# Kernel tuning notes

Hardware: AMD Instinct MI355X
Metric: run time of the kernel (lower is better)

The kernel has to match this reference:

```python
import jax, jax.numpy as jnp
import numpy as np

B, D, H, O, E = 16384, 1024, 512, 256, 8


def setup_inputs() -> dict:
    key = jax.random.key(0)
    ks = jax.random.split(key, 8)
    s = lambda k, shape, fan: (jax.random.normal(k, shape, jnp.float32) / np.sqrt(fan).astype(np.float32))
    z = lambda shape: jnp.zeros(shape, jnp.float32)
    return {
        "x": jax.random.normal(ks[0], (B, D), jnp.float32),
        # gating network: D -> 256 -> 128 -> E
        "gw1": s(ks[1], (D, 256), D), "gb1": z((256,)),
        "gw2": s(ks[2], (256, 128), 256), "gb2": z((128,)),
        "gw3": s(ks[3], (128, E), 128), "gb3": z((E,)),
        # experts, batched over expert dim E: D -> H -> H -> O
        "ew1": s(ks[4], (E, D, H), D), "eb1": z((E, H)),
        "ew2": s(ks[5], (E, H, H), H), "eb2": z((E, H)),
        "ew3": s(ks[6], (E, H, O), H), "eb3": z((E, O)),
    }


def reference(x, gw1, gb1, gw2, gb2, gw3, gb3, ew1, eb1, ew2, eb2, ew3, eb3):
    # Gating network (dropout is identity in eval mode)
    g = jax.nn.relu(x @ gw1 + gb1)
    g = jax.nn.relu(g @ gw2 + gb2)
    gates = jax.nn.softmax(g @ gw3 + gb3, axis=1)  # [B, E]
    # All experts run on every token: batched small MLPs over expert axis e
    h = jax.nn.relu(jnp.einsum('bd,edh->ebh', x, ew1) + eb1[:, None, :])   # [E, B, H]
    h = jax.nn.relu(jnp.einsum('ebh,ehk->ebk', h, ew2) + eb2[:, None, :])  # [E, B, H]
    eo = jnp.einsum('ebh,eho->ebo', h, ew3) + eb3[:, None, :]              # [E, B, O]
    # gate-weighted sum over experts
    out = jnp.einsum('ebo,be->bo', eo, gates)  # [B, O]
    return out
```

## Files before the change

kernel.cpp:

```cpp
#include <hip/hip_runtime.h>
#include <hip/hip_bf16.h>

typedef __hip_bfloat16 bf16;
typedef __attribute__((ext_vector_type(8))) __bf16 bf16x8;
typedef __attribute__((ext_vector_type(4))) float f32x4;

#define B_ 16384
#define D_ 1024
#define H_ 512
#define O_ 256
#define E_ 8
#define BC_ 8192

static_assert(B_ % BC_ == 0, "chunking");

#define GLDS(src, dst) __builtin_amdgcn_global_load_lds( \
    (const __attribute__((address_space(1))) void*)(src), \
    (__attribute__((address_space(3))) void*)(dst), 16, 0, 0)

#define BAR()   asm volatile("s_barrier" ::: "memory")
#define LGKM0() do { asm volatile("s_waitcnt lgkmcnt(0)" ::: "memory"); \
                     __builtin_amdgcn_sched_barrier(0); } while (0)

__global__ void detect_k(const unsigned short* __restrict__ x, int* __restrict__ flag) {
    __shared__ int s;
    if (threadIdx.x == 0) s = 0;
    __syncthreads();
    int big = 0;
    for (int i = threadIdx.x; i < 2048; i += 256)
        if (((x[i] >> 7) & 0xFF) >= 150) big = 1;
    if (big) atomicOr(&s, 1);
    __syncthreads();
    if (threadIdx.x == 0) *flag = s;
}

__global__ void cvt_k(const void* __restrict__ src, bf16* __restrict__ dst,
                      const int* __restrict__ flag, long n) {
    const int f = *flag;
    long i = (long)blockIdx.x * blockDim.x + threadIdx.x;
    const long stride = (long)gridDim.x * blockDim.x;
    if (f) {
        const float* s = (const float*)src;
        for (; i < n; i += stride) dst[i] = __float2bfloat16(s[i]);
    } else {
        const bf16* s = (const bf16*)src;
        for (; i < n; i += stride) dst[i] = s[i];
    }
}

__global__ void transpose_k(const void* __restrict__ in, bf16* __restrict__ out,
                            const int* __restrict__ flag, int R, int C,
                            long z_out, long c_stride) {
    __shared__ bf16 t[32][33];
    const int f = *flag;
    const long zi = (long)blockIdx.z * R * C;
    const int x = blockIdx.x * 32 + threadIdx.x;
    const int y0 = blockIdx.y * 32;
    const float* inf = (const float*)in;
    const bf16* inb = (const bf16*)in;
#pragma unroll
    for (int i = 0; i < 4; i++) {
        int r = y0 + threadIdx.y + i * 8;
        long idx = zi + (long)r * C + x;
        t[threadIdx.y + i * 8][threadIdx.x] =
            f ? __float2bfloat16(inf[idx]) : inb[idx];
    }
    __syncthreads();
    const int xr = blockIdx.y * 32 + threadIdx.x;
    const long zo = (long)blockIdx.z * z_out;
#pragma unroll
    for (int i = 0; i < 4; i++) {
        int c = blockIdx.x * 32 + threadIdx.y + i * 8;
        out[zo + (long)c * c_stride + xr] = t[threadIdx.x][threadIdx.y + i * 8];
    }
}

__global__ void gate3_softmax_k(const bf16* __restrict__ g2,
                                const bf16* __restrict__ gw3,
                                const bf16* __restrict__ gb3,
                                float* __restrict__ gates) {
    __shared__ float w[128 * 8];
    __shared__ float bsh[8];
    const int tid = threadIdx.x;
    for (int i = tid; i < 1024; i += 256) w[i] = __bfloat162float(gw3[i]);
    if (tid < 8) bsh[tid] = __bfloat162float(gb3[tid]);
    __syncthreads();

    const long row = (long)blockIdx.x * 256 + tid;
    float acc[8];
#pragma unroll
    for (int o = 0; o < 8; o++) acc[o] = bsh[o];

    const bf16x8* rp8 = (const bf16x8*)(g2 + row * 128);
#pragma unroll 4
    for (int c8 = 0; c8 < 16; c8++) {
        bf16x8 v8 = rp8[c8];
#pragma unroll
        for (int jj = 0; jj < 8; jj++) {
            float v = (float)v8[jj];
            int k = c8 * 8 + jj;
#pragma unroll
            for (int o = 0; o < 8; o++) acc[o] += v * w[k * 8 + o];
        }
    }
    float m = acc[0];
#pragma unroll
    for (int o = 1; o < 8; o++) m = fmaxf(m, acc[o]);
    float s = 0.f;
#pragma unroll
    for (int o = 0; o < 8; o++) { acc[o] = __expf(acc[o] - m); s += acc[o]; }
    const float inv = 1.f / s;
#pragma unroll
    for (int o = 0; o < 8; o++) gates[row * 8 + o] = acc[o] * inv;
}

template <int MODE>
__global__ __launch_bounds__(256, 4)
void gemm_bt(const bf16* __restrict__ A, const bf16* __restrict__ Bt,
             const bf16* __restrict__ bias, const float* __restrict__ gates,
             void* __restrict__ Cout, const bf16* __restrict__ eb3,
             const int* __restrict__ oflag,
             int lda, int ldb, int ldo, int K,
             long a_z, long b_z, long bias_z, long out_z,
             int e_gate, int k_per_e, long a_e, long b_e, long row0) {
    __shared__ __attribute__((aligned(16))) bf16 As[128 * 32];
    __shared__ __attribute__((aligned(16))) bf16 Bs[128 * 32];

    const int tid  = threadIdx.x;
    const int lane = tid & 63;
    const int quad = lane >> 4;
    const int l15  = lane & 15;
    const int wid  = tid >> 6;
    const int wr   = (wid >> 1) << 6;
    const int wc   = (wid & 1) << 6;
    const int z    = blockIdx.z;
    const long m0  = (long)blockIdx.y << 7;
    const long n0  = (long)blockIdx.x << 7;

    const bf16* Az = A + (long)z * a_z;
    const bf16* Bz = Bt + (long)z * b_z;

    f32x4 acc[4][4];
#pragma unroll
    for (int i = 0; i < 4; i++)
#pragma unroll
        for (int j = 0; j < 4; j++) acc[i][j] = (f32x4){0.f, 0.f, 0.f, 0.f};

    const int erow = tid >> 2;
    const int ecol = (tid & 3) << 3;

    const int n_e   = k_per_e ? (K / k_per_e) : 1;
    const int inner = (k_per_e ? k_per_e : K) >> 5;

    for (int e = 0; e < n_e; e++) {
        const bf16* Ae = Az + (long)e * a_e;
        const bf16* Be = Bz + (long)e * b_e;
        for (int kti = 0; kti < inner; kti++) {
            const int kk = kti << 5;
#pragma unroll
            for (int i = 0; i < 2; i++) {
                const int r = (i << 6) + erow;
                GLDS(Ae + (m0 + r) * lda + (kk + ecol), As + r * 32 + ecol);
            }
#pragma unroll
            for (int i = 0; i < 2; i++) {
                const int r = (i << 6) + erow;
                GLDS(Be + (n0 + r) * ldb + (kk + ecol), Bs + r * 32 + ecol);
            }
            __syncthreads();
            bf16x8 af[4], bfr[4];
#pragma unroll
            for (int i = 0; i < 4; i++)
                af[i] = *(const bf16x8*)(As + (wr + i * 16 + l15) * 32 + (quad << 3));
#pragma unroll
            for (int j = 0; j < 4; j++)
                bfr[j] = *(const bf16x8*)(Bs + (wc + j * 16 + l15) * 32 + (quad << 3));
#pragma unroll
            for (int i = 0; i < 4; i++)
#pragma unroll
                for (int j = 0; j < 4; j++)
                    acc[i][j] = __builtin_amdgcn_mfma_f32_16x16x32_bf16(
                        af[i], bfr[j], acc[i][j], 0, 0, 0);
            __syncthreads();
        }
    }

    const int eg = (e_gate >= 0) ? e_gate : z;

    if constexpr (MODE == 0 || MODE == 1) {
        bf16* C = (bf16*)Cout + (long)z * out_z;
        const bf16* bb = bias + (long)z * bias_z;
        float gv[4][4];
        if constexpr (MODE == 1) {
#pragma unroll
            for (int i = 0; i < 4; i++)
#pragma unroll
                for (int rg = 0; rg < 4; rg++)
                    gv[i][rg] = gates[(row0 + m0 + wr + i * 16 + quad * 4 + rg) * 8 + eg];
        }
#pragma unroll
        for (int j = 0; j < 4; j++) {
            const int c = (int)n0 + wc + j * 16 + l15;
            const float bv = __bfloat162float(bb[c]);
#pragma unroll
            for (int i = 0; i < 4; i++) {
#pragma unroll
                for (int rg = 0; rg < 4; rg++) {
                    const long r = m0 + wr + i * 16 + quad * 4 + rg;
                    float v = fmaxf(acc[i][j][rg] + bv, 0.f);
                    if constexpr (MODE == 1) v *= gv[i][rg];
                    C[r * ldo + c] = __float2bfloat16(v);
                }
            }
        }
    } else if constexpr (MODE == 2) {
        float* C = (float*)Cout;
#pragma unroll
        for (int i = 0; i < 4; i++) {
#pragma unroll
            for (int rg = 0; rg < 4; rg++) {
                const long r = m0 + wr + i * 16 + quad * 4 + rg;
                const float g = gates[(row0 + r) * 8 + eg];
#pragma unroll
                for (int j = 0; j < 4; j++) {
                    const int c = (int)n0 + wc + j * 16 + l15;
                    const float b3 = __bfloat162float(eb3[eg * O_ + c]);
                    C[r * ldo + c] += acc[i][j][rg] + g * b3;
                }
            }
        }
    }
}

template <int MODE>
__global__ __launch_bounds__(512, 2)
void gemm256(const bf16* __restrict__ A, const bf16* __restrict__ Bt,
             const bf16* __restrict__ bias, const float* __restrict__ gates,
             void* __restrict__ Cout, const bf16* __restrict__ eb3,
             int lda, int ldb, int ldo, int K,
             long a_z, long b_z, long bias_z, long out_z, long row0) {
    __shared__ __attribute__((aligned(16))) bf16 lds[2][2][256 * 64];

    int bx = blockIdx.x, by = blockIdx.y;
    {
        const int gx = gridDim.x;
        const int nwg = gx * gridDim.y;
        if ((nwg & 7) == 0) {
            int lin = bx + gx * by;
            lin = (lin & 7) * (nwg >> 3) + (lin >> 3);
            bx = lin % gx; by = lin / gx;
        }
    }

    const int tid  = threadIdx.x;
    const int lane = tid & 63;
    const int quad = lane >> 4;
    const int l15  = lane & 15;
    const int w    = tid >> 6;
    const int wm   = w >> 2;
    const int wn   = w & 3;
    const int z    = blockIdx.z;
    const long m0  = (long)by << 8;
    const long n0  = (long)bx << 8;

    const bf16* __restrict__ Az = A + z * a_z;
    const bf16* __restrict__ Bz = Bt + z * b_z;

    f32x4 acc[8][4];
#pragma unroll
    for (int i = 0; i < 8; ++i)
#pragma unroll
        for (int j = 0; j < 4; ++j) acc[i][j] = (f32x4){0.f, 0.f, 0.f, 0.f};

    bf16x8 af[4][2], bv[2][2];

    auto stage = [&](int buf, int mat, int half, int kt) {
        const bf16* __restrict__ G = mat ? Bz : Az;
        const int ld = mat ? ldb : lda;
        const long p0 = mat ? n0 : m0;
#pragma unroll
        for (int l = 0; l < 2; ++l) {
            const int ci = (w << 1) | l;
            const int rb = mat ? ((ci >> 2) << 6) + (half << 5) + ((ci & 3) << 3)
                               : ((ci >> 3) << 7) + (half << 6) + ((ci & 7) << 3);
            const int row = rb + (lane >> 3);
            const int cb  = ((lane & 7) << 4) ^ ((row & 7) << 4);
            GLDS(G + (p0 + row) * ld + kt * 64 + (cb >> 1),
                 &lds[buf][mat][rb * 64]);
        }
    };
    auto ldaf = [&](int buf, int qm) {
#pragma unroll
        for (int i = 0; i < 4; ++i) {
            const int r = (wm << 7) + (qm << 6) + (i << 4) + l15;
            const char* p = (const char*)&lds[buf][0][r * 64];
            const int sw = (r & 7) << 4;
#pragma unroll
            for (int s = 0; s < 2; ++s)
                af[i][s] = *(const bf16x8*)(p + (((s << 6) + (quad << 4)) ^ sw));
        }
    };
    auto ldbf = [&](int buf, int qn) {
#pragma unroll
        for (int j = 0; j < 2; ++j) {
            const int r = (wn << 6) + (qn << 5) + (j << 4) + l15;
            const char* p = (const char*)&lds[buf][1][r * 64];
            const int sw = (r & 7) << 4;
#pragma unroll
            for (int s = 0; s < 2; ++s)
                bv[j][s] = *(const bf16x8*)(p + (((s << 6) + (quad << 4)) ^ sw));
        }
    };
    auto mmac = [&](int qm, int qn) {
#pragma unroll
        for (int i = 0; i < 4; ++i)
#pragma unroll
            for (int j = 0; j < 2; ++j)
#pragma unroll
                for (int s = 0; s < 2; ++s)
                    acc[(qm << 2) + i][(qn << 1) + j] =
                        __builtin_amdgcn_mfma_f32_16x16x32_bf16(
                            af[i][s], bv[j][s], acc[(qm << 2) + i][(qn << 1) + j],
                            0, 0, 0);
    };

    const int nt = K >> 6;

    stage(0, 0, 0, 0); stage(0, 0, 1, 0); stage(0, 1, 0, 0); stage(0, 1, 1, 0);
    stage(1, 0, 0, 1); stage(1, 1, 0, 1);
    asm volatile("s_waitcnt vmcnt(4)" ::: "memory");
    BAR();

    const int hi = nt >> 1;
    for (int it = 0; it < hi; ++it) {
        const int t1k = 2 * it + 1, t2k = 2 * it + 2, t3k = 2 * it + 3;
        const bool do2 = t2k < nt, do3 = t3k < nt;
        ldaf(0, 0); ldbf(0, 0); stage(1, 0, 1, t1k);
        BAR(); LGKM0();
        __builtin_amdgcn_s_setprio(1); mmac(0, 0); __builtin_amdgcn_s_setprio(0);
        BAR();
        ldbf(0, 1); stage(1, 1, 1, t1k);
        BAR(); LGKM0();
        __builtin_amdgcn_s_setprio(1); mmac(0, 1); __builtin_amdgcn_s_setprio(0);
        BAR();
        ldaf(0, 1); ldbf(0, 0); if (do2) stage(0, 0, 0, t2k);
        BAR(); LGKM0();
        __builtin_amdgcn_s_setprio(1); mmac(1, 0); __builtin_amdgcn_s_setprio(0);
        BAR();
        ldbf(0, 1); if (do2) stage(0, 1, 0, t2k);
        BAR(); LGKM0();
        __builtin_amdgcn_s_setprio(1); mmac(1, 1); __builtin_amdgcn_s_setprio(0);
        if (do2) { asm volatile("s_waitcnt vmcnt(4)" ::: "memory"); }
        else     { asm volatile("s_waitcnt vmcnt(0)" ::: "memory"); }
        BAR();
        ldaf(1, 0); ldbf(1, 0); if (do2) stage(0, 0, 1, t2k);
        BAR(); LGKM0();
        __builtin_amdgcn_s_setprio(1); mmac(0, 0); __builtin_amdgcn_s_setprio(0);
        BAR();
        ldbf(1, 1); if (do2) stage(0, 1, 1, t2k);
        BAR(); LGKM0();
        __builtin_amdgcn_s_setprio(1); mmac(0, 1); __builtin_amdgcn_s_setprio(0);
        BAR();
        ldaf(1, 1); ldbf(1, 0); if (do3) stage(1, 0, 0, t3k);
        BAR(); LGKM0();
        __builtin_amdgcn_s_setprio(1); mmac(1, 0); __builtin_amdgcn_s_setprio(0);
        BAR();
        ldbf(1, 1); if (do3) stage(1, 1, 0, t3k);
        BAR(); LGKM0();
        __builtin_amdgcn_s_setprio(1); mmac(1, 1); __builtin_amdgcn_s_setprio(0);
        if (do3) { asm volatile("s_waitcnt vmcnt(4)" ::: "memory"); }
        else     { asm volatile("s_waitcnt vmcnt(0)" ::: "memory"); }
        BAR();
    }

    if constexpr (MODE == 0 || MODE == 1) {
        bf16* C = (bf16*)Cout + z * out_z;
        const bf16* bb = bias + z * bias_z;
        float bvv[4];
#pragma unroll
        for (int jg = 0; jg < 4; ++jg)
            bvv[jg] = __bfloat162float(bb[(int)n0 + (wn << 6) + (jg << 4) + l15]);
#pragma unroll
        for (int ig = 0; ig < 8; ++ig) {
#pragma unroll
            for (int rg = 0; rg < 4; ++rg) {
                const long r = m0 + (wm << 7) + (ig << 4) + (quad << 2) + rg;
                float g = 1.f;
                if constexpr (MODE == 1) g = gates[(row0 + r) * 8 + z];
#pragma unroll
                for (int jg = 0; jg < 4; ++jg) {
                    const int c = (int)n0 + (wn << 6) + (jg << 4) + l15;
                    float v = fmaxf(acc[ig][jg][rg] + bvv[jg], 0.f);
                    if constexpr (MODE == 1) v *= g;
                    C[r * ldo + c] = __float2bfloat16(v);
                }
            }
        }
    } else {
        float* C = (float*)Cout + z * out_z;
        float b3v[4];
#pragma unroll
        for (int jg = 0; jg < 4; ++jg)
            b3v[jg] = __bfloat162float(eb3[z * O_ + (int)n0 + (wn << 6) + (jg << 4) + l15]);
#pragma unroll
        for (int ig = 0; ig < 8; ++ig) {
#pragma unroll
            for (int rg = 0; rg < 4; ++rg) {
                const long r = m0 + (wm << 7) + (ig << 4) + (quad << 2) + rg;
                const float g = gates[(row0 + r) * 8 + z];
#pragma unroll
                for (int jg = 0; jg < 4; ++jg) {
                    const int c = (int)n0 + (wn << 6) + (jg << 4) + l15;
                    C[r * ldo + c] = acc[ig][jg][rg] + g * b3v[jg];
                }
            }
        }
    }
}

__global__ void zero_f32_k(float* __restrict__ p) {
    p[(long)blockIdx.x * 256 + threadIdx.x] = 0.f;
}
__global__ void out_cvt_k(const float* __restrict__ in, void* __restrict__ out,
                          const int* __restrict__ flag) {
    const long i = (long)blockIdx.x * 256 + threadIdx.x;
    if (*flag) ((float*)out)[i] = in[i];
    else       ((bf16*)out)[i] = __float2bfloat16(in[i]);
}
__global__ void reduce8_k(const float* __restrict__ p, void* __restrict__ out,
                          const int* __restrict__ flag, long off) {
    const long n = (long)BC_ * O_;
    const long i = ((long)blockIdx.x * 256 + threadIdx.x) * 4;
    float4 s = *(const float4*)(p + i);
#pragma unroll
    for (int zz = 1; zz < 8; ++zz) {
        float4 a = *(const float4*)(p + (long)zz * n + i);
        s.x += a.x; s.y += a.y; s.z += a.z; s.w += a.w;
    }
    if (*flag) {
        *(float4*)((float*)out + off + i) = s;
    } else {
        bf16* o = (bf16*)out + off + i;
        o[0] = __float2bfloat16(s.x); o[1] = __float2bfloat16(s.y);
        o[2] = __float2bfloat16(s.z); o[3] = __float2bfloat16(s.w);
    }
}

extern "C" void kernel_launch(void* const* d_in, const int* in_sizes, int n_in,
                              void* d_out, int out_size, void* d_ws, size_t ws_size,
                              hipStream_t stream) {
    (void)in_sizes; (void)n_in; (void)out_size;
    const void* x   = d_in[0];
    const void* gw1 = d_in[1];
    const void* gb1 = d_in[2];
    const void* gw2 = d_in[3];
    const void* gb2 = d_in[4];
    const void* gw3 = d_in[5];
    const void* gb3 = d_in[6];
    const void* ew1 = d_in[7];
    const void* eb1 = d_in[8];
    const void* ew2 = d_in[9];
    const void* eb2 = d_in[10];
    const void* ew3 = d_in[11];
    const void* eb3 = d_in[12];

    char* ws = (char*)d_ws;
    size_t off = 0;
    auto alloc = [&](size_t n) { char* p = ws + off; off += (n + 255) & ~(size_t)255; return p; };

    int*  flag  = (int*)alloc(256);
    bf16* xc    = (bf16*)alloc((size_t)B_ * D_ * 2);
    bf16* gw1t  = (bf16*)alloc((size_t)256 * 1024 * 2);
    bf16* gw2t  = (bf16*)alloc((size_t)128 * 256 * 2);
    bf16* ew1t  = (bf16*)alloc((size_t)E_ * H_ * D_ * 2);
    bf16* ew2t  = (bf16*)alloc((size_t)E_ * H_ * H_ * 2);
    bf16* ew3t  = (bf16*)alloc((size_t)E_ * O_ * H_ * 2);
    bf16* gb1c  = (bf16*)alloc(256 * 2);
    bf16* gb2c  = (bf16*)alloc(128 * 2);
    bf16* gw3c  = (bf16*)alloc(1024 * 2);
    bf16* gb3c  = (bf16*)alloc(8 * 2);
    bf16* eb1c  = (bf16*)alloc((size_t)E_ * H_ * 2);
    bf16* eb2c  = (bf16*)alloc((size_t)E_ * H_ * 2);
    bf16* eb3c  = (bf16*)alloc((size_t)E_ * O_ * 2);
    bf16* g1    = (bf16*)alloc((size_t)B_ * 256 * 2);
    bf16* g2b   = (bf16*)alloc((size_t)B_ * 128 * 2);
    float* gates = (float*)alloc((size_t)B_ * 8 * 4);

    const size_t small = off;
    const size_t needA = small + ((size_t)E_ * BC_ * H_ * 2 + 256)
                               + ((size_t)BC_ * E_ * H_ * 2 + 256)
                               + (8ull * BC_ * O_ * 4 + 256) + 4096;
    const bool pathA = ws_size >= needA;

    detect_k<<<1, 256, 0, stream>>>((const unsigned short*)x, flag);

    cvt_k<<<4096, 256, 0, stream>>>(x, xc, flag, (long)B_ * D_);
    cvt_k<<<1, 256, 0, stream>>>(gb1, gb1c, flag, 256);
    cvt_k<<<1, 256, 0, stream>>>(gb2, gb2c, flag, 128);
    cvt_k<<<4, 256, 0, stream>>>(gw3, gw3c, flag, 1024);
    cvt_k<<<1, 256, 0, stream>>>(gb3, gb3c, flag, 8);
    cvt_k<<<16, 256, 0, stream>>>(eb1, eb1c, flag, (long)E_ * H_);
    cvt_k<<<16, 256, 0, stream>>>(eb2, eb2c, flag, (long)E_ * H_);
    cvt_k<<<8, 256, 0, stream>>>(eb3, eb3c, flag, (long)E_ * O_);

    transpose_k<<<dim3(256 / 32, 1024 / 32, 1), dim3(32, 8), 0, stream>>>(
        gw1, gw1t, flag, 1024, 256, 0L, 1024L);
    transpose_k<<<dim3(128 / 32, 256 / 32, 1), dim3(32, 8), 0, stream>>>(
        gw2, gw2t, flag, 256, 128, 0L, 256L);
    transpose_k<<<dim3(H_ / 32, D_ / 32, E_), dim3(32, 8), 0, stream>>>(
        ew1, ew1t, flag, D_, H_, (long)H_ * D_, (long)D_);
    transpose_k<<<dim3(H_ / 32, H_ / 32, E_), dim3(32, 8), 0, stream>>>(
        ew2, ew2t, flag, H_, H_, (long)H_ * H_, (long)H_);
    if (pathA)
        transpose_k<<<dim3(O_ / 32, H_ / 32, E_), dim3(32, 8), 0, stream>>>(
            ew3, ew3t, flag, H_, O_, (long)H_, (long)E_ * H_);
    else
        transpose_k<<<dim3(O_ / 32, H_ / 32, E_), dim3(32, 8), 0, stream>>>(
            ew3, ew3t, flag, H_, O_, (long)O_ * H_, (long)H_);

    gemm_bt<0><<<dim3(2, 128, 1), 256, 0, stream>>>(
        xc, gw1t, gb1c, nullptr, g1, nullptr, nullptr,
        1024, 1024, 256, 1024, 0, 0, 0, 0, 0, 0, 0, 0, 0);
    gemm_bt<0><<<dim3(1, 128, 1), 256, 0, stream>>>(
        g1, gw2t, gb2c, nullptr, g2b, nullptr, nullptr,
        256, 256, 128, 256, 0, 0, 0, 0, 0, 0, 0, 0, 0);
    gate3_softmax_k<<<dim3(B_ / 256), 256, 0, stream>>>(g2b, gw3c, gb3c, gates);

    if (pathA) {
        bf16* h1c   = (bf16*)alloc((size_t)E_ * BC_ * H_ * 2);
        bf16* h2    = (bf16*)alloc((size_t)BC_ * E_ * H_ * 2);
        float* parts = (float*)alloc(8ull * BC_ * O_ * 4);
        for (int ch = 0; ch < B_ / BC_; ch++) {
            const long rb = (long)ch * BC_;
            gemm256<0><<<dim3(2, BC_ / 256, 8), 512, 0, stream>>>(
                xc + rb * D_, ew1t, eb1c, nullptr, h1c, nullptr,
                D_, D_, H_, D_,
                0, (long)H_ * D_, (long)H_, (long)BC_ * H_, 0);
            gemm256<1><<<dim3(2, BC_ / 256, 8), 512, 0, stream>>>(
                h1c, ew2t, eb2c, gates, h2, nullptr,
                H_, H_, E_ * H_, H_,
                (long)BC_ * H_, (long)H_ * H_, (long)H_, (long)H_, rb);
            gemm256<4><<<dim3(1, BC_ / 256, 8), 512, 0, stream>>>(
                h2, ew3t, nullptr, gates, parts, eb3c,
                E_ * H_, E_ * H_, O_, 512,
                (long)H_, (long)H_, 0, (long)BC_ * O_, rb);
            reduce8_k<<<dim3(BC_ * O_ / 1024), 256, 0, stream>>>(
                parts, d_out, flag, rb * O_);
        }
    } else {
        bf16* h1s = (bf16*)alloc((size_t)B_ * H_ * 2);
        bf16* h2s = (bf16*)alloc((size_t)B_ * H_ * 2);
        float* oacc = (float*)alloc((size_t)B_ * O_ * 4);
        zero_f32_k<<<dim3(B_ * O_ / 256), 256, 0, stream>>>(oacc);
        for (int e = 0; e < E_; e++) {
            gemm_bt<0><<<dim3(4, 128, 1), 256, 0, stream>>>(
                xc, ew1t + (size_t)e * H_ * D_, eb1c + (size_t)e * H_, nullptr, h1s, nullptr, nullptr,
                1024, 1024, 512, 1024, 0, 0, 0, 0, 0, 0, 0, 0, 0);
            gemm_bt<1><<<dim3(4, 128, 1), 256, 0, stream>>>(
                h1s, ew2t + (size_t)e * H_ * H_, eb2c + (size_t)e * H_, gates, h2s, nullptr, nullptr,
                512, 512, 512, 512, 0, 0, 0, 0, e, 0, 0, 0, 0);
            gemm_bt<2><<<dim3(2, 128, 1), 256, 0, stream>>>(
                h2s, ew3t + (size_t)e * O_ * H_, nullptr, gates, oacc, eb3c, nullptr,
                512, 512, 256, 512, 0, 0, 0, 0, e, 0, 0, 0, 0);
        }
        out_cvt_k<<<dim3(B_ * O_ / 256), 256, 0, stream>>>(oacc, d_out, flag);
    }
}
```

Before: 547.7 us.

## Fuse pairs of experts per GEMM block and batch layer-3 across chunks

The expert GEMM kernel now walks several expert segments along K in one launch, running a per-segment epilogue mid-loop. Each block handles two experts, so the grid z-dimension is halved for layers 1 and 2. When workspace allows, layer 3 runs once over the full batch with four partial outputs and a 4-way reduce instead of per-chunk 8-way partials. The small conversion kernels are merged into one launch and the x conversion is vectorised. This cuts launch count, partial-sum traffic and reduce work, at the cost of extra epilogue work inside the main loop and larger h2 and parts buffers.

```diff
diff --git a/kernel.cpp b/kernel.cpp
--- a/kernel.cpp
+++ b/kernel.cpp
@@ -34,18 +34,44 @@
     if (threadIdx.x == 0) *flag = s;
 }
 
-__global__ void cvt_k(const void* __restrict__ src, bf16* __restrict__ dst,
-                      const int* __restrict__ flag, long n) {
+__global__ void cvtx_k(const void* __restrict__ src, bf16* __restrict__ dst,
+                       const int* __restrict__ flag, long n8) {
     const int f = *flag;
     long i = (long)blockIdx.x * blockDim.x + threadIdx.x;
     const long stride = (long)gridDim.x * blockDim.x;
     if (f) {
-        const float* s = (const float*)src;
-        for (; i < n; i += stride) dst[i] = __float2bfloat16(s[i]);
+        const float4* s = (const float4*)src;
+        for (; i < n8; i += stride) {
+            float4 a = s[2 * i], b = s[2 * i + 1];
+            bf16 tmp[8];
+            tmp[0] = __float2bfloat16(a.x); tmp[1] = __float2bfloat16(a.y);
+            tmp[2] = __float2bfloat16(a.z); tmp[3] = __float2bfloat16(a.w);
+            tmp[4] = __float2bfloat16(b.x); tmp[5] = __float2bfloat16(b.y);
+            tmp[6] = __float2bfloat16(b.z); tmp[7] = __float2bfloat16(b.w);
+            *(uint4*)(dst + i * 8) = *(const uint4*)tmp;
+        }
     } else {
-        const bf16* s = (const bf16*)src;
-        for (; i < n; i += stride) dst[i] = s[i];
-    }
+        const uint4* s = (const uint4*)src;
+        for (; i < n8; i += stride) *(uint4*)(dst + i * 8) = s[i];
+    }
+}
+
+__global__ void small_cvt_k(const void* s0, const void* s1, const void* s2,
+                            const void* s3, const void* s4, const void* s5,
+                            const void* s6,
+                            bf16* d0, bf16* d1, bf16* d2, bf16* d3,
+                            bf16* d4, bf16* d5, bf16* d6,
+                            const int* __restrict__ flag) {
+    const int f = *flag;
+    const int id = blockIdx.x;
+    const void* sp[7] = {s0, s1, s2, s3, s4, s5, s6};
+    bf16* dp[7] = {d0, d1, d2, d3, d4, d5, d6};
+    const int len[7] = {256, 128, 1024, 8, E_ * H_, E_ * H_, E_ * O_};
+    const float* sf = (const float*)sp[id];
+    const bf16*  sb = (const bf16*)sp[id];
+    bf16* d = dp[id];
+    for (int i = threadIdx.x; i < len[id]; i += 256)
+        d[i] = f ? __float2bfloat16(sf[i]) : sb[i];
 }
 
 __global__ void transpose_k(const void* __restrict__ in, bf16* __restrict__ out,
@@ -237,8 +263,9 @@
 void gemm256(const bf16* __restrict__ A, const bf16* __restrict__ Bt,
              const bf16* __restrict__ bias, const float* __restrict__ gates,
              void* __restrict__ Cout, const bf16* __restrict__ eb3,
-             int lda, int ldb, int ldo, int K,
-             long a_z, long b_z, long bias_z, long out_z, long row0) {
+             int lda, int ldb, int ldo, int nseg, int ksh,
+             long a_z, long a_s, long b_e, long bias_e,
+             long out_e, long out_z, long row0) {
     __shared__ __attribute__((aligned(16))) bf16 lds[2][2][256 * 64];
 
     int bx = blockIdx.x, by = blockIdx.y;
@@ -263,9 +290,6 @@
     const long m0  = (long)by << 8;
     const long n0  = (long)bx << 8;
 
-    const bf16* __restrict__ Az = A + z * a_z;
-    const bf16* __restrict__ Bz = Bt + z * b_z;
-
     f32x4 acc[8][4];
 #pragma unroll
     for (int i = 0; i < 8; ++i)
@@ -274,8 +298,16 @@
 
     bf16x8 af[4][2], bv[2][2];
 
+    const int ntseg = 1 << ksh;
+    const int nt    = nseg << ksh;
+    const int seghi = 1 << (ksh - 1);
+
     auto stage = [&](int buf, int mat, int half, int kt) {
-        const bf16* __restrict__ G = mat ? Bz : Az;
+        const int seg = kt >> ksh;
+        const int ktl = kt & (ntseg - 1);
+        const long e  = (long)z * nseg + seg;
+        const bf16* __restrict__ G =
+            mat ? (Bt + e * b_e) : (A + (long)z * a_z + (long)seg * a_s);
         const int ld = mat ? ldb : lda;
         const long p0 = mat ? n0 : m0;
 #pragma unroll
@@ -285,7 +317,7 @@
                                : ((ci >> 3) << 7) + (half << 6) + ((ci & 7) << 3);
             const int row = rb + (lane >> 3);
             const int cb  = ((lane & 7) << 4) ^ ((row & 7) << 4);
-            GLDS(G + (p0 + row) * ld + kt * 64 + (cb >> 1),
+            GLDS(G + (p0 + row) * ld + ktl * 64 + (cb >> 1),
                  &lds[buf][mat][rb * 64]);
         }
     };
@@ -323,59 +355,10 @@
                             af[i][s], bv[j][s], acc[(qm << 2) + i][(qn << 1) + j],
                             0, 0, 0);
     };
-
-    const int nt = K >> 6;
-
-    stage(0, 0, 0, 0); stage(0, 0, 1, 0); stage(0, 1, 0, 0); stage(0, 1, 1, 0);
-    stage(1, 0, 0, 1); stage(1, 1, 0, 1);
-    asm volatile("s_waitcnt vmcnt(4)" ::: "memory");
-    BAR();
-
-    const int hi = nt >> 1;
-    for (int it = 0; it < hi; ++it) {
-        const int t1k = 2 * it + 1, t2k = 2 * it + 2, t3k = 2 * it + 3;
-        const bool do2 = t2k < nt, do3 = t3k < nt;
-        ldaf(0, 0); ldbf(0, 0); stage(1, 0, 1, t1k);
-        BAR(); LGKM0();
-        __builtin_amdgcn_s_setprio(1); mmac(0, 0); __builtin_amdgcn_s_setprio(0);
-        BAR();
-        ldbf(0, 1); stage(1, 1, 1, t1k);
-        BAR(); LGKM0();
-        __builtin_amdgcn_s_setprio(1); mmac(0, 1); __builtin_amdgcn_s_setprio(0);
-        BAR();
-        ldaf(0, 1); ldbf(0, 0); if (do2) stage(0, 0, 0, t2k);
-        BAR(); LGKM0();
-        __builtin_amdgcn_s_setprio(1); mmac(1, 0); __builtin_amdgcn_s_setprio(0);
-        BAR();
-        ldbf(0, 1); if (do2) stage(0, 1, 0, t2k);
-        BAR(); LGKM0();
-        __builtin_amdgcn_s_setprio(1); mmac(1, 1); __builtin_amdgcn_s_setprio(0);
-        if (do2) { asm volatile("s_waitcnt vmcnt(4)" ::: "memory"); }
-        else     { asm volatile("s_waitcnt vmcnt(0)" ::: "memory"); }
-        BAR();
-        ldaf(1, 0); ldbf(1, 0); if (do2) stage(0, 0, 1, t2k);
-        BAR(); LGKM0();
-        __builtin_amdgcn_s_setprio(1); mmac(0, 0); __builtin_amdgcn_s_setprio(0);
-        BAR();
-        ldbf(1, 1); if (do2) stage(0, 1, 1, t2k);
-        BAR(); LGKM0();
-        __builtin_amdgcn_s_setprio(1); mmac(0, 1); __builtin_amdgcn_s_setprio(0);
-        BAR();
-        ldaf(1, 1); ldbf(1, 0); if (do3) stage(1, 0, 0, t3k);
-        BAR(); LGKM0();
-        __builtin_amdgcn_s_setprio(1); mmac(1, 0); __builtin_amdgcn_s_setprio(0);
-        BAR();
-        ldbf(1, 1); if (do3) stage(1, 1, 0, t3k);
-        BAR(); LGKM0();
-        __builtin_amdgcn_s_setprio(1); mmac(1, 1); __builtin_amdgcn_s_setprio(0);
-        if (do3) { asm volatile("s_waitcnt vmcnt(4)" ::: "memory"); }
-        else     { asm volatile("s_waitcnt vmcnt(0)" ::: "memory"); }
-        BAR();
-    }
-
-    if constexpr (MODE == 0 || MODE == 1) {
-        bf16* C = (bf16*)Cout + z * out_z;
-        const bf16* bb = bias + z * bias_z;
+    auto epi01 = [&](int s) {
+        const long e = (long)z * nseg + s;
+        bf16* C = (bf16*)Cout + e * out_e;
+        const bf16* bb = bias + e * bias_e;
         float bvv[4];
 #pragma unroll
         for (int jg = 0; jg < 4; ++jg)
@@ -386,7 +369,7 @@
             for (int rg = 0; rg < 4; ++rg) {
                 const long r = m0 + (wm << 7) + (ig << 4) + (quad << 2) + rg;
                 float g = 1.f;
-                if constexpr (MODE == 1) g = gates[(row0 + r) * 8 + z];
+                if constexpr (MODE == 1) g = gates[(row0 + r) * 8 + e];
 #pragma unroll
                 for (int jg = 0; jg < 4; ++jg) {
                     const int c = (int)n0 + (wn << 6) + (jg << 4) + l15;
@@ -396,22 +379,84 @@
                 }
             }
         }
+#pragma unroll
+        for (int i = 0; i < 8; ++i)
+#pragma unroll
+            for (int j = 0; j < 4; ++j) acc[i][j] = (f32x4){0.f, 0.f, 0.f, 0.f};
+    };
+
+    stage(0, 0, 0, 0); stage(0, 0, 1, 0); stage(0, 1, 0, 0); stage(0, 1, 1, 0);
+    stage(1, 0, 0, 1); stage(1, 1, 0, 1);
+    asm volatile("s_waitcnt vmcnt(4)" ::: "memory");
+    BAR();
+
+    const int hi = nt >> 1;
+    for (int it = 0; it < hi; ++it) {
+        const int t1k = 2 * it + 1, t2k = 2 * it + 2, t3k = 2 * it + 3;
+        const bool do2 = t2k < nt, do3 = t3k < nt;
+        ldaf(0, 0); ldbf(0, 0); stage(1, 0, 1, t1k);
+        BAR(); LGKM0();
+        __builtin_amdgcn_s_setprio(1); mmac(0, 0); __builtin_amdgcn_s_setprio(0);
+        BAR();
+        ldbf(0, 1); stage(1, 1, 1, t1k);
+        BAR(); LGKM0();
+        __builtin_amdgcn_s_setprio(1); mmac(0, 1); __builtin_amdgcn_s_setprio(0);
+        BAR();
+        ldaf(0, 1); ldbf(0, 0); if (do2) stage(0, 0, 0, t2k);
+        BAR(); LGKM0();
+        __builtin_amdgcn_s_setprio(1); mmac(1, 0); __builtin_amdgcn_s_setprio(0);
+        BAR();
+        ldbf(0, 1); if (do2) stage(0, 1, 0, t2k);
+        BAR(); LGKM0();
+        __builtin_amdgcn_s_setprio(1); mmac(1, 1); __builtin_amdgcn_s_setprio(0);
+        if (do2) { asm volatile("s_waitcnt vmcnt(4)" ::: "memory"); }
+        else     { asm volatile("s_waitcnt vmcnt(0)" ::: "memory"); }
+        BAR();
+        ldaf(1, 0); ldbf(1, 0); if (do2) stage(0, 0, 1, t2k);
+        BAR(); LGKM0();
+        __builtin_amdgcn_s_setprio(1); mmac(0, 0); __builtin_amdgcn_s_setprio(0);
+        BAR();
+        ldbf(1, 1); if (do2) stage(0, 1, 1, t2k);
+        BAR(); LGKM0();
+        __builtin_amdgcn_s_setprio(1); mmac(0, 1); __builtin_amdgcn_s_setprio(0);
+        BAR();
+        ldaf(1, 1); ldbf(1, 0); if (do3) stage(1, 0, 0, t3k);
+        BAR(); LGKM0();
+        __builtin_amdgcn_s_setprio(1); mmac(1, 0); __builtin_amdgcn_s_setprio(0);
+        BAR();
+        ldbf(1, 1); if (do3) stage(1, 1, 0, t3k);
+        BAR(); LGKM0();
+        __builtin_amdgcn_s_setprio(1); mmac(1, 1); __builtin_amdgcn_s_setprio(0);
+        if (do3) { asm volatile("s_waitcnt vmcnt(4)" ::: "memory"); }
+        else     { asm volatile("s_waitcnt vmcnt(0)" ::: "memory"); }
+        BAR();
+        if constexpr (MODE == 0 || MODE == 1) {
+            if (nseg > 1 && ((it + 1) & (seghi - 1)) == 0) {
+                const int s = ((it + 1) >> (ksh - 1)) - 1;
+                if (s < nseg - 1) epi01(s);
+            }
+        }
+    }
+
+    if constexpr (MODE == 0 || MODE == 1) {
+        epi01(nseg - 1);
     } else {
-        float* C = (float*)Cout + z * out_z;
-        float b3v[4];
-#pragma unroll
-        for (int jg = 0; jg < 4; ++jg)
-            b3v[jg] = __bfloat162float(eb3[z * O_ + (int)n0 + (wn << 6) + (jg << 4) + l15]);
+        float* C = (float*)Cout + (long)z * out_z;
 #pragma unroll
         for (int ig = 0; ig < 8; ++ig) {
 #pragma unroll
             for (int rg = 0; rg < 4; ++rg) {
                 const long r = m0 + (wm << 7) + (ig << 4) + (quad << 2) + rg;
-                const float g = gates[(row0 + r) * 8 + z];
 #pragma unroll
                 for (int jg = 0; jg < 4; ++jg) {
                     const int c = (int)n0 + (wn << 6) + (jg << 4) + l15;
-                    C[r * ldo + c] = acc[ig][jg][rg] + g * b3v[jg];
+                    float v = acc[ig][jg][rg];
+                    for (int s = 0; s < nseg; ++s) {
+                        const long e = (long)z * nseg + s;
+                        v += gates[(row0 + r) * 8 + e] *
+                             __bfloat162float(eb3[e * O_ + c]);
+                    }
+                    C[r * ldo + c] = v;
                 }
             }
         }
@@ -427,13 +472,13 @@
     if (*flag) ((float*)out)[i] = in[i];
     else       ((bf16*)out)[i] = __float2bfloat16(in[i]);
 }
-__global__ void reduce8_k(const float* __restrict__ p, void* __restrict__ out,
-                          const int* __restrict__ flag, long off) {
-    const long n = (long)BC_ * O_;
+template <int NZ>
+__global__ void reduceN_k(const float* __restrict__ p, void* __restrict__ out,
+                          const int* __restrict__ flag, long n, long off) {
     const long i = ((long)blockIdx.x * 256 + threadIdx.x) * 4;
     float4 s = *(const float4*)(p + i);
 #pragma unroll
-    for (int zz = 1; zz < 8; ++zz) {
+    for (int zz = 1; zz < NZ; ++zz) {
         float4 a = *(const float4*)(p + (long)zz * n + i);
         s.x += a.x; s.y += a.y; s.z += a.z; s.w += a.w;
     }
@@ -487,21 +532,21 @@
     float* gates = (float*)alloc((size_t)B_ * 8 * 4);
 
     const size_t small = off;
-    const size_t needA = small + ((size_t)E_ * BC_ * H_ * 2 + 256)
-                               + ((size_t)BC_ * E_ * H_ * 2 + 256)
-                               + (8ull * BC_ * O_ * 4 + 256) + 4096;
-    const bool pathA = ws_size >= needA;
+    const size_t needMid = small + ((size_t)E_ * BC_ * H_ * 2 + 256)
+                                 + ((size_t)B_ * E_ * H_ * 2 + 256)
+                                 + (4ull * B_ * O_ * 4 + 256) + 4096;
+    const size_t needChunk = small + ((size_t)E_ * BC_ * H_ * 2 + 256)
+                                   + ((size_t)BC_ * E_ * H_ * 2 + 256)
+                                   + (8ull * BC_ * O_ * 4 + 256) + 4096;
+    const bool pathMid   = ws_size >= needMid;
+    const bool pathChunk = ws_size >= needChunk;
 
     detect_k<<<1, 256, 0, stream>>>((const unsigned short*)x, flag);
 
-    cvt_k<<<4096, 256, 0, stream>>>(x, xc, flag, (long)B_ * D_);
-    cvt_k<<<1, 256, 0, stream>>>(gb1, gb1c, flag, 256);
-    cvt_k<<<1, 256, 0, stream>>>(gb2, gb2c, flag, 128);
-    cvt_k<<<4, 256, 0, stream>>>(gw3, gw3c, flag, 1024);
-    cvt_k<<<1, 256, 0, stream>>>(gb3, gb3c, flag, 8);
-    cvt_k<<<16, 256, 0, stream>>>(eb1, eb1c, flag, (long)E_ * H_);
-    cvt_k<<<16, 256, 0, stream>>>(eb2, eb2c, flag, (long)E_ * H_);
-    cvt_k<<<8, 256, 0, stream>>>(eb3, eb3c, flag, (long)E_ * O_);
+    cvtx_k<<<2048, 256, 0, stream>>>(x, xc, flag, (long)B_ * D_ / 8);
+    small_cvt_k<<<7, 256, 0, stream>>>(gb1, gb2, gw3, gb3, eb1, eb2, eb3,
+                                       gb1c, gb2c, gw3c, gb3c, eb1c, eb2c, eb3c,
+                                       flag);
 
     transpose_k<<<dim3(256 / 32, 1024 / 32, 1), dim3(32, 8), 0, stream>>>(
         gw1, gw1t, flag, 1024, 256, 0L, 1024L);
@@ -511,7 +556,7 @@
         ew1, ew1t, flag, D_, H_, (long)H_ * D_, (long)D_);
     transpose_k<<<dim3(H_ / 32, H_ / 32, E_), dim3(32, 8), 0, stream>>>(
         ew2, ew2t, flag, H_, H_, (long)H_ * H_, (long)H_);
-    if (pathA)
+    if (pathChunk)
         transpose_k<<<dim3(O_ / 32, H_ / 32, E_), dim3(32, 8), 0, stream>>>(
             ew3, ew3t, flag, H_, O_, (long)H_, (long)E_ * H_);
     else
@@ -526,26 +571,43 @@
         256, 256, 128, 256, 0, 0, 0, 0, 0, 0, 0, 0, 0);
     gate3_softmax_k<<<dim3(B_ / 256), 256, 0, stream>>>(g2b, gw3c, gb3c, gates);
 
-    if (pathA) {
-        bf16* h1c   = (bf16*)alloc((size_t)E_ * BC_ * H_ * 2);
-        bf16* h2    = (bf16*)alloc((size_t)BC_ * E_ * H_ * 2);
-        float* parts = (float*)alloc(8ull * BC_ * O_ * 4);
+    if (pathChunk) {
+        bf16* h1c = (bf16*)alloc((size_t)E_ * BC_ * H_ * 2);
+        bf16* h2  = pathMid
+                  ? (bf16*)alloc((size_t)B_ * E_ * H_ * 2)
+                  : (bf16*)alloc((size_t)BC_ * E_ * H_ * 2);
+        float* parts = pathMid
+                     ? (float*)alloc(4ull * B_ * O_ * 4)
+                     : (float*)alloc(8ull * BC_ * O_ * 4);
+
         for (int ch = 0; ch < B_ / BC_; ch++) {
             const long rb = (long)ch * BC_;
-            gemm256<0><<<dim3(2, BC_ / 256, 8), 512, 0, stream>>>(
+            gemm256<0><<<dim3(2, BC_ / 256, 4), 512, 0, stream>>>(
                 xc + rb * D_, ew1t, eb1c, nullptr, h1c, nullptr,
-                D_, D_, H_, D_,
-                0, (long)H_ * D_, (long)H_, (long)BC_ * H_, 0);
-            gemm256<1><<<dim3(2, BC_ / 256, 8), 512, 0, stream>>>(
-                h1c, ew2t, eb2c, gates, h2, nullptr,
-                H_, H_, E_ * H_, H_,
-                (long)BC_ * H_, (long)H_ * H_, (long)H_, (long)H_, rb);
-            gemm256<4><<<dim3(1, BC_ / 256, 8), 512, 0, stream>>>(
+                D_, D_, H_, 2, 4,
+                0L, 0L, (long)H_ * D_, (long)H_, (long)BC_ * H_, 0L, 0L);
+            bf16* h2dst = pathMid ? (h2 + rb * (long)E_ * H_) : h2;
+            gemm256<1><<<dim3(2, BC_ / 256, 4), 512, 0, stream>>>(
+                h1c, ew2t, eb2c, gates, h2dst, nullptr,
+                H_, H_, E_ * H_, 2, 3,
+                2L * BC_ * H_, (long)BC_ * H_, (long)H_ * H_, (long)H_,
+                (long)H_, 0L, rb);
+            if (!pathMid) {
+                gemm256<4><<<dim3(1, BC_ / 256, 8), 512, 0, stream>>>(
+                    h2, ew3t, nullptr, gates, parts, eb3c,
+                    E_ * H_, E_ * H_, O_, 1, 3,
+                    512L, 0L, 512L, 0L, 0L, (long)BC_ * O_, rb);
+                reduceN_k<8><<<dim3(BC_ * O_ / 1024), 256, 0, stream>>>(
+                    parts, d_out, flag, (long)BC_ * O_, rb * O_);
+            }
+        }
+        if (pathMid) {
+            gemm256<4><<<dim3(1, B_ / 256, 4), 512, 0, stream>>>(
                 h2, ew3t, nullptr, gates, parts, eb3c,
-                E_ * H_, E_ * H_, O_, 512,
-                (long)H_, (long)H_, 0, (long)BC_ * O_, rb);
-            reduce8_k<<<dim3(BC_ * O_ / 1024), 256, 0, stream>>>(
-                parts, d_out, flag, rb * O_);
+                E_ * H_, E_ * H_, O_, 2, 3,
+                1024L, 512L, 512L, 0L, 0L, (long)B_ * O_, 0L);
+            reduceN_k<4><<<dim3(B_ * O_ / 1024), 256, 0, stream>>>(
+                parts, d_out, flag, (long)B_ * O_, 0L);
         }
     } else {
         bf16* h1s = (bf16*)alloc((size_t)B_ * H_ * 2);
```

Measured after the change: 733.3 us. 1.34x slower.
